# Kernel optimization log

Measured on AMD Instinct MI355X. Metric: run time of the kernel, lower is better.

## Reference

```python
import jax, jax.numpy as jnp
import numpy as np

N, E, D, O, M = 50000, 800000, 128, 128, 2

def _wn(x, v, g, b):
    # weight_norm linear: W = g * v / ||v||_row ; y = x @ W.T + b
    w = g * v / jnp.linalg.norm(v, axis=1, keepdims=True)
    return x @ w.T + b

def _gelu(x):
    return jax.nn.gelu(x, approximate=False)  # torch F.gelu default is exact erf

def setup_inputs() -> dict:
    key = jax.random.key(0)
    ks = jax.random.split(key, 32)
    inp = {"feat": jax.random.normal(ks[0], (N, D), jnp.float32)}
    layers = [("asrc", D, O), ("adst", D, O), ("asub", D, O), ("amul", D, O), ("aout", O, 1),
              ("pool", D, D), ("pool2", D, D), ("self", D, O), ("neigh", D, O), ("neigh2", D, O)]
    for i, (nm, fi, fo) in enumerate(layers):
        inp[nm + "_v"] = jax.random.normal(ks[i + 1], (fo, fi), jnp.float32) * (1.0 / np.sqrt(fi))
        inp[nm + "_g"] = jnp.ones((fo, 1), jnp.float32)
        inp[nm + "_b"] = jnp.zeros((fo,), jnp.float32)
    inp["mlp_v"] = jax.random.normal(ks[20], (M, O, O), jnp.float32) * (1.0 / np.sqrt(O))
    inp["mlp_g"] = jnp.ones((M, O, 1), jnp.float32)
    inp["mlp_b"] = jnp.zeros((M, O), jnp.float32)
    inp["src"] = jax.random.randint(ks[21], (E,), 0, N)
    inp["dst"] = jax.random.randint(ks[22], (E,), 0, N)
    return inp

def reference(feat, asrc_v, asrc_g, asrc_b, adst_v, adst_g, adst_b,
              asub_v, asub_g, asub_b, amul_v, amul_g, amul_b,
              aout_v, aout_g, aout_b, pool_v, pool_g, pool_b,
              pool2_v, pool2_g, pool2_b, self_v, self_g, self_b,
              neigh_v, neigh_g, neigh_b, neigh2_v, neigh2_g, neigh2_b,
              mlp_v, mlp_g, mlp_b, src, dst):
    fs, fd = feat[src], feat[dst]                        # [E, D] gathers
    e = (_wn(fs - fd, asub_v, asub_g, asub_b)
         + _wn(fs * fd, amul_v, amul_g, amul_b)
         + _wn(feat, asrc_v, asrc_g, asrc_b)[src]
         + _wn(feat, adst_v, adst_g, adst_b)[dst])       # [E, O]
    e = _gelu(e)
    e = jax.nn.leaky_relu(_wn(e, aout_v, aout_g, aout_b), 0.2)  # [E, 1] attention scalar

    cnt = jax.ops.segment_sum(jnp.ones((E,), feat.dtype), dst, num_segments=N)[:, None]  # in-degree

    h = _gelu(_wn(feat, pool_v, pool_g, pool_b))         # [N, D]
    neigh = jax.ops.segment_max(e * h[src], dst, num_segments=N)
    neigh = jnp.where(cnt > 0, neigh, jnp.zeros_like(neigh))  # zero for isolated dst nodes

    h2 = _gelu(_wn(feat, pool2_v, pool2_g, pool2_b))
    neigh2 = jax.ops.segment_sum(e * h2[src], dst, num_segments=N) / jnp.maximum(cnt, 1.0)

    rst = (_wn(feat, self_v, self_g, self_b)
           + _wn(neigh, neigh_v, neigh_g, neigh_b)
           + _wn(neigh2, neigh2_v, neigh2_g, neigh2_b))
    for i in range(M):
        rst = rst + _wn(_gelu(rst), mlp_v[i], mlp_g[i], mlp_b[i])
    return rst
```

## Files before the change

kernel.cpp:

```cpp
#include <hip/hip_runtime.h>
#include <hip/hip_bf16.h>
#include <math.h>

constexpr int NN = 50000;
constexpr int EE = 800000;

constexpr int OFF_WT_NODE  = 0;
constexpr int OFF_WT_AMUL  = 65536;
constexpr int OFF_WT_FINAL = 81920;
constexpr int OFF_WT_MLP   = 131072;
constexpr int OFF_WAOUT    = 163840;
constexpr int OFF_BE       = 163968;
constexpr int OFF_BFIN     = 164096;
constexpr int OFF_BAOUT    = 164224;
constexpr int OFF_WNODEBF  = 164240;
constexpr int OFF_WFINBF   = OFF_WNODEBF + 32768;
constexpr int OFF_WMLPBF   = OFF_WFINBF + 24576;
constexpr int OFF_WAMULBF  = OFF_WMLPBF + 16384;
constexpr int OFF_FEATBF   = OFF_WAMULBF + 8192;
constexpr int OFF_SBF      = OFF_FEATBF + NN*64;
constexpr int OFF_WEDGEBF  = OFF_SBF;
constexpr int OFF_HBF      = OFF_SBF + NN*128;
constexpr int OFF_SEV      = OFF_HBF + NN*128;
constexpr int OFF_NEIGHBF  = OFF_SEV + EE;
constexpr int OFF_STARTS   = OFF_NEIGHBF + NN*128;
constexpr int OFF_HIST     = OFF_STARTS + NN + 8;
constexpr int OFF_CURSOR   = OFF_HIST + NN;
constexpr int OFF_SSRCD    = OFF_CURSOR + NN;

constexpr int SCAN_NB = (NN + 255) / 256;

typedef __attribute__((ext_vector_type(8))) _Float16 f16x8;
typedef __attribute__((ext_vector_type(2))) _Float16 f16x2;
typedef __attribute__((ext_vector_type(2))) __fp16 fp16x2r;
typedef __attribute__((ext_vector_type(4))) float f32x4;

__device__ __forceinline__ float gelu_f(float x) {
    float x2 = x * x;
    float w = x * fmaf(-0.1029448f, x2, -2.3022082f);
    return x * __builtin_amdgcn_rcpf(1.0f + __builtin_amdgcn_exp2f(w));
}
__device__ __forceinline__ float leaky_f(float x) {
    return x > 0.0f ? x : 0.2f * x;
}
__device__ __forceinline__ unsigned pk_f16(float lo, float hi) {
    fp16x2r p = __builtin_amdgcn_cvt_pkrtz(lo, hi);
    return *reinterpret_cast<unsigned*>(&p);
}
__device__ __forceinline__ unsigned short f2h(float x) {
    fp16x2r p = __builtin_amdgcn_cvt_pkrtz(x, 0.0f);
    return *reinterpret_cast<unsigned short*>(&p);
}
__device__ __forceinline__ unsigned mulpack_h(unsigned a, unsigned b) {
    f16x2 x = *reinterpret_cast<f16x2*>(&a);
    f16x2 y = *reinterpret_cast<f16x2*>(&b);
    f16x2 r = x * y;
    return *reinterpret_cast<unsigned*>(&r);
}
__device__ __forceinline__ float2 up2(unsigned u) {
    f16x2 p = *reinterpret_cast<f16x2*>(&u);
    return make_float2((float)p.x, (float)p.y);
}
__device__ __forceinline__ float block_sum128(float v, float* sbuf) {
    #pragma unroll
    for (int o = 32; o > 0; o >>= 1) v += __shfl_down(v, o, 64);
    int lane = threadIdx.x & 63, w = threadIdx.x >> 6;
    if (lane == 0) sbuf[w] = v;
    __syncthreads();
    float r = sbuf[0] + sbuf[1];
    __syncthreads();
    return r;
}

struct WnormArgs {
    const float *asrc_v, *asrc_g, *asrc_b;
    const float *adst_v, *adst_g, *adst_b;
    const float *asub_v, *asub_g, *asub_b;
    const float *amul_v, *amul_g, *amul_b;
    const float *aout_v, *aout_g, *aout_b;
    const float *pool_v, *pool_g, *pool_b;
    const float *pool2_v, *pool2_g, *pool2_b;
    const float *self_v, *self_g, *self_b;
    const float *neigh_v, *neigh_g, *neigh_b;
    const float *neigh2_v, *neigh2_g, *neigh2_b;
    const float *mlp_v, *mlp_g, *mlp_b;
    float* ws;
};

__global__ __launch_bounds__(128) void wnorm_kernel(WnormArgs a) {
    __shared__ float sbuf[2];
    int bid = blockIdx.x, i = threadIdx.x;
    float* ws = a.ws;
    int gid = bid * 128 + i;
    if (gid < NN) ((int*)(ws + OFF_HIST))[gid] = 0;
    if (bid < 1280) {
        int o = bid & 127, grp = bid >> 7;
        const float *v1 = nullptr, *g1 = nullptr, *v2 = nullptr, *g2 = nullptr;
        float sgn2 = 1.0f; float* dst = nullptr; int stride = 0;
        switch (grp) {
            case 0: v1=a.asrc_v; g1=a.asrc_g; v2=a.asub_v; g2=a.asub_g; sgn2= 1.f; dst=ws+OFF_WT_NODE+o;        stride=512; break;
            case 1: v1=a.adst_v; g1=a.adst_g; v2=a.asub_v; g2=a.asub_g; sgn2=-1.f; dst=ws+OFF_WT_NODE+128+o;    stride=512; break;
            case 2: v1=a.pool_v;  g1=a.pool_g;  dst=ws+OFF_WT_NODE+256+o;          stride=512; break;
            case 3: v1=a.pool2_v; g1=a.pool2_g; dst=ws+OFF_WT_NODE+384+o;          stride=512; break;
            case 4: v1=a.amul_v;  g1=a.amul_g;  dst=ws+OFF_WT_AMUL+o;              stride=128; break;
            case 5: v1=a.neigh_v; g1=a.neigh_g; dst=ws+OFF_WT_FINAL+o;             stride=128; break;
            case 6: v1=a.neigh2_v;g1=a.neigh2_g;dst=ws+OFF_WT_FINAL+128*128+o;     stride=128; break;
            case 7: v1=a.self_v;  g1=a.self_g;  dst=ws+OFF_WT_FINAL+256*128+o;     stride=128; break;
            case 8: v1=a.mlp_v;        g1=a.mlp_g;     dst=ws+OFF_WT_MLP+o;        stride=128; break;
            case 9: v1=a.mlp_v+16384;  g1=a.mlp_g+128; dst=ws+OFF_WT_MLP+16384+o;  stride=128; break;
        }
        float x1 = v1[o*128 + i];
        float n1 = sqrtf(block_sum128(x1*x1, sbuf));
        float w = g1[o] * x1 / n1;
        if (v2) {
            float x2 = v2[o*128 + i];
            float n2 = sqrtf(block_sum128(x2*x2, sbuf));
            w += sgn2 * g2[o] * x2 / n2;
        }
        dst[i * stride] = w;
    } else {
        float v = a.aout_v[i];
        float n = sqrtf(block_sum128(v*v, sbuf));
        ws[OFF_WAOUT + i] = a.aout_g[0] * v / n;
        ws[OFF_BE + i]    = a.asrc_b[i] + a.adst_b[i] + a.asub_b[i] + a.amul_b[i];
        ws[OFF_BFIN + i]  = a.self_b[i] + a.neigh_b[i] + a.neigh2_b[i];
        if (i == 0) ws[OFF_BAOUT] = a.aout_b[0];
    }
}

__global__ __launch_bounds__(256) void convert_weights_kernel(float* __restrict__ ws) {
    int idx = blockIdx.x * 256 + threadIdx.x;
    unsigned short* wnodebf = (unsigned short*)(ws + OFF_WNODEBF);
    unsigned short* wfinbf  = (unsigned short*)(ws + OFF_WFINBF);
    unsigned short* wmlpbf  = (unsigned short*)(ws + OFF_WMLPBF);
    unsigned short* wedgebf = (unsigned short*)(ws + OFF_WEDGEBF);
    if (idx < 65536) {
        int k = idx >> 9, n = idx & 511;
        wnodebf[n * 128 + k] = f2h(ws[OFF_WT_NODE + k * 512 + n]);
    } else if (idx < 114688) {
        int i = idx - 65536, k = i >> 7, o = i & 127;
        wfinbf[o * 384 + k] = f2h(ws[OFF_WT_FINAL + k * 128 + o]);
    } else if (idx < 147456) {
        int i = idx - 114688, l = i >> 14, j = i & 16383, k = j >> 7, o = j & 127;
        wmlpbf[l * 16384 + o * 128 + k] = f2h(ws[OFF_WT_MLP + l * 16384 + k * 128 + o]);
    } else {
        int i = idx - 147456;
        int elem = i & 7, f = i >> 3;
        int lane = f & 63, kb = (f >> 6) & 3, ts = f >> 8;
        int t = ts / 3, slice = ts - t * 3;
        int o = t * 16 + (lane & 15);
        int kk = kb * 32 + (lane >> 4) * 8 + elem;
        float v = (slice == 0) ? ws[OFF_WT_AMUL + kk * 128 + o]
                : (slice == 1) ? ws[OFF_WT_NODE + kk * 512 + o]
                               : ws[OFF_WT_NODE + kk * 512 + 128 + o];
        wedgebf[i] = f2h(v);
    }
}

__global__ __launch_bounds__(256) void hist_kernel(const int* __restrict__ dst, float* __restrict__ ws) {
    int e = blockIdx.x * 256 + threadIdx.x;
    if (e < EE) atomicAdd(&((int*)(ws + OFF_HIST))[dst[e]], 1);
}

__global__ __launch_bounds__(256) void scan_blocks_kernel(float* __restrict__ ws) {
    __shared__ int wsum[4];
    const int* hist = (const int*)(ws + OFF_HIST);
    int* starts = (int*)(ws + OFF_STARTS);
    int* bsum = (int*)(ws + OFF_SEV);
    int bid = blockIdx.x, t = threadIdx.x;
    int idx = bid * 256 + t;
    int lane = t & 63, w = t >> 6;
    int v = (idx < NN) ? hist[idx] : 0;
    int s = v;
    #pragma unroll
    for (int o = 1; o < 64; o <<= 1) {
        int u = __shfl_up(s, o, 64);
        if (lane >= o) s += u;
    }
    if (lane == 63) wsum[w] = s;
    __syncthreads();
    int off = 0;
    for (int i = 0; i < w; ++i) off += wsum[i];
    int incl = s + off;
    if (idx < NN) starts[idx] = incl - v;
    if (t == 255) bsum[bid] = incl;
}

__global__ __launch_bounds__(256) void scan_add_kernel(float* __restrict__ ws) {
    __shared__ int sb4[4];
    int* starts = (int*)(ws + OFF_STARTS);
    int* cursor = (int*)(ws + OFF_CURSOR);
    const int* bsum = (const int*)(ws + OFF_SEV);
    int bid = blockIdx.x, t = threadIdx.x;
    int lane = t & 63, w = t >> 6;
    int v = (t < bid) ? bsum[t] : 0;
    int s = v;
    #pragma unroll
    for (int o = 32; o > 0; o >>= 1) s += __shfl_down(s, o, 64);
    if (lane == 0) sb4[w] = s;
    __syncthreads();
    int prefix = sb4[0] + sb4[1] + sb4[2] + sb4[3];
    int idx = bid * 256 + t;
    if (idx < NN) {
        int sv = starts[idx] + prefix;
        starts[idx] = sv;
        cursor[idx] = sv;
    }
    if (idx == 0) starts[NN] = EE;
}

__global__ __launch_bounds__(256) void scatteridx_kernel(const int* __restrict__ src,
                                                         const int* __restrict__ dst,
                                                         float* __restrict__ ws) {
    int e = blockIdx.x * 256 + threadIdx.x;
    if (e >= EE) return;
    int d = dst[e];
    int pos = atomicAdd(&((int*)(ws + OFF_CURSOR))[d], 1);
    ((int2*)(ws + OFF_SSRCD))[pos] = make_int2(src[e], d);
}

__global__ __launch_bounds__(256) void segreduce_kernel(float* __restrict__ ws) {
    int n = blockIdx.x * 4 + (threadIdx.x >> 6);
    int lane = threadIdx.x & 63;
    const int* starts = (const int*)(ws + OFF_STARTS);
    const int2* ssrcd = (const int2*)(ws + OFF_SSRCD);
    const float* sev = ws + OFF_SEV;
    const unsigned short* hbf = (const unsigned short*)(ws + OFF_HBF);
    unsigned short* neighbf = (unsigned short*)(ws + OFF_NEIGHBF);
    int s0 = starts[n], s1 = starts[n + 1];
    float2 mx = make_float2(-INFINITY, -INFINITY);
    float2 sm = make_float2(0.f, 0.f);
    int i = s0;
    for (; i + 4 <= s1; i += 4) {
        int sA = ssrcd[i].x, sB = ssrcd[i + 1].x, sC = ssrcd[i + 2].x, sD = ssrcd[i + 3].x;
        float eA = sev[i], eB = sev[i + 1], eC = sev[i + 2], eD = sev[i + 3];
        uint2 vA = *(const uint2*)&hbf[sA * 256 + lane * 4];
        uint2 vB = *(const uint2*)&hbf[sB * 256 + lane * 4];
        uint2 vC = *(const uint2*)&hbf[sC * 256 + lane * 4];
        uint2 vD = *(const uint2*)&hbf[sD * 256 + lane * 4];
        float2 hA = up2(vA.x), gA = up2(vA.y);
        float2 hB = up2(vB.x), gB = up2(vB.y);
        float2 hC = up2(vC.x), gC = up2(vC.y);
        float2 hD = up2(vD.x), gD = up2(vD.y);
        mx.x = fmaxf(mx.x, eA * hA.x); mx.y = fmaxf(mx.y, eA * hA.y);
        sm.x += eA * gA.x;             sm.y += eA * gA.y;
        mx.x = fmaxf(mx.x, eB * hB.x); mx.y = fmaxf(mx.y, eB * hB.y);
        sm.x += eB * gB.x;             sm.y += eB * gB.y;
        mx.x = fmaxf(mx.x, eC * hC.x); mx.y = fmaxf(mx.y, eC * hC.y);
        sm.x += eC * gC.x;             sm.y += eC * gC.y;
        mx.x = fmaxf(mx.x, eD * hD.x); mx.y = fmaxf(mx.y, eD * hD.y);
        sm.x += eD * gD.x;             sm.y += eD * gD.y;
    }
    for (; i < s1; ++i) {
        int s = ssrcd[i].x;
        float ev = sev[i];
        uint2 v = *(const uint2*)&hbf[s * 256 + lane * 4];
        float2 h = up2(v.x), g = up2(v.y);
        mx.x = fmaxf(mx.x, ev * h.x); mx.y = fmaxf(mx.y, ev * h.y);
        sm.x += ev * g.x;             sm.y += ev * g.y;
    }
    int cnt = s1 - s0;
    if (cnt == 0) { mx.x = 0.f; mx.y = 0.f; }
    float ic = 1.0f / (float)max(cnt, 1);
    *(unsigned*)&neighbf[n * 256 + lane * 2] = pk_f16(mx.x, mx.y);
    *(unsigned*)&neighbf[n * 256 + 128 + lane * 2] = pk_f16(sm.x * ic, sm.y * ic);
}

__global__ __launch_bounds__(256) void gemm_node_mfma(const float* __restrict__ feat,
                                                      const float* __restrict__ pool_b,
                                                      const float* __restrict__ pool2_b,
                                                      unsigned short* __restrict__ featbf,
                                                      unsigned short* __restrict__ hbf,
                                                      const unsigned short* __restrict__ wnodebf) {
    __shared__ unsigned short As[64 * 136];
    int tid = threadIdx.x;
    int row0 = blockIdx.x * 64;
    #pragma unroll
    for (int it = 0; it < 8; ++it) {
        int idx = tid + it * 256;
        int r = idx >> 5, u = idx & 31;
        int rr = min(row0 + r, NN - 1);
        float4 v = ((const float4*)feat)[rr * 32 + u];
        unsigned p0 = pk_f16(v.x, v.y);
        unsigned p1 = pk_f16(v.z, v.w);
        *(unsigned*)&As[r * 136 + u * 4]     = p0;
        *(unsigned*)&As[r * 136 + u * 4 + 2] = p1;
        *(uint2*)&featbf[rr * 128 + u * 4] = make_uint2(p0, p1);
    }
    __syncthreads();
    int lane = tid & 63, w = tid >> 6;
    int quad = lane >> 4, l15 = lane & 15;
    #pragma unroll 1
    for (int gy = 0; gy < 2; ++gy) {
        const unsigned short* B = wnodebf + (gy + 2) * 128 * 128;
        const float* bias = gy == 0 ? pool_b : pool2_b;
        f32x4 acc[8] = {};
        #pragma unroll 1
        for (int ks = 0; ks < 4; ++ks) {
            f16x8 a = *(const f16x8*)&As[(w * 16 + l15) * 136 + ks * 32 + quad * 8];
            #pragma unroll
            for (int t = 0; t < 8; ++t) {
                f16x8 b = *(const f16x8*)&B[(t * 16 + l15) * 128 + ks * 32 + quad * 8];
                acc[t] = __builtin_amdgcn_mfma_f32_16x16x32_f16(a, b, acc[t], 0, 0, 0);
            }
        }
        #pragma unroll
        for (int reg = 0; reg < 4; ++reg) {
            int row = row0 + w * 16 + quad * 4 + reg;
            if (row >= NN) continue;
            #pragma unroll
            for (int t = 0; t < 8; ++t) {
                int col = t * 16 + l15;
                hbf[row * 256 + ((col >> 1) << 2) + (col & 1) + gy * 2] =
                    f2h(gelu_f(acc[t][reg] + bias[col]));
            }
        }
    }
}

__global__ __launch_bounds__(256, 3) void gemm_edge(const unsigned short* __restrict__ featbf,
                                                    const unsigned short* __restrict__ wedgebf,
                                                    float* __restrict__ ws) {
    __shared__ unsigned short Bs[2][24 * 512];
    int tid = threadIdx.x;
    int lane = tid & 63, w = tid >> 6;
    int quad = lane >> 4, l15 = lane & 15;
    int e0 = blockIdx.x * 128;
    const int2* ssrcd = (const int2*)(ws + OFF_SSRCD);
    int base = e0 + w * 32 + l15;
    int2 i0 = ssrcd[base];
    int2 i1 = ssrcd[base + 16];
    const unsigned short* p0s = &featbf[i0.x * 128];
    const unsigned short* p0d = &featbf[i0.y * 128];
    const unsigned short* p1s = &featbf[i1.x * 128];
    const unsigned short* p1d = &featbf[i1.y * 128];
    int ko = quad * 8;

    uint4 ca[2][4];
    ca[0][0] = *(const uint4*)&p0s[ko];
    ca[0][1] = *(const uint4*)&p0d[ko];
    ca[0][2] = *(const uint4*)&p1s[ko];
    ca[0][3] = *(const uint4*)&p1d[ko];
    ca[1][0] = *(const uint4*)&p0s[ko + 32];
    ca[1][1] = *(const uint4*)&p0d[ko + 32];
    ca[1][2] = *(const uint4*)&p1s[ko + 32];
    ca[1][3] = *(const uint4*)&p1d[ko + 32];
    uint4 sb[6];
    #pragma unroll
    for (int i = 0; i < 6; ++i) {
        int ts = w * 6 + i;
        sb[i] = *(const uint4*)&wedgebf[(ts * 4 + 0) * 512 + lane * 8];
    }
    #pragma unroll
    for (int i = 0; i < 6; ++i) {
        int ts = w * 6 + i;
        *(uint4*)&Bs[0][ts * 512 + lane * 8] = sb[i];
    }
    __syncthreads();

    f32x4 acc0[8] = {}, acc1[8] = {};
    #pragma unroll
    for (int kb = 0; kb < 4; ++kb) {
        uint4 c0s = ca[kb & 1][0], c0d = ca[kb & 1][1];
        uint4 c1s = ca[kb & 1][2], c1d = ca[kb & 1][3];
        uint4 m0, m1;
        m0.x = mulpack_h(c0s.x, c0d.x); m0.y = mulpack_h(c0s.y, c0d.y);
        m0.z = mulpack_h(c0s.z, c0d.z); m0.w = mulpack_h(c0s.w, c0d.w);
        m1.x = mulpack_h(c1s.x, c1d.x); m1.y = mulpack_h(c1s.y, c1d.y);
        m1.z = mulpack_h(c1s.z, c1d.z); m1.w = mulpack_h(c1s.w, c1d.w);
        f16x8 am0 = *(const f16x8*)&m0,  am1 = *(const f16x8*)&m1;
        f16x8 as0 = *(const f16x8*)&c0s, ad0 = *(const f16x8*)&c0d;
        f16x8 as1 = *(const f16x8*)&c1s, ad1 = *(const f16x8*)&c1d;
        if (kb < 2) {
            int k2 = ko + (kb + 2) * 32;
            ca[kb & 1][0] = *(const uint4*)&p0s[k2];
            ca[kb & 1][1] = *(const uint4*)&p0d[k2];
            ca[kb & 1][2] = *(const uint4*)&p1s[k2];
            ca[kb & 1][3] = *(const uint4*)&p1d[k2];
        }
        if (kb < 3) {
            #pragma unroll
            for (int i = 0; i < 6; ++i) {
                int ts = w * 6 + i;
                sb[i] = *(const uint4*)&wedgebf[(ts * 4 + kb + 1) * 512 + lane * 8];
            }
        }
        const unsigned short* bb = &Bs[kb & 1][lane * 8];
        #pragma unroll
        for (int t = 0; t < 8; ++t) {
            f16x8 bm = *(const f16x8*)&bb[(t * 3 + 0) * 512];
            f16x8 b1 = *(const f16x8*)&bb[(t * 3 + 1) * 512];
            f16x8 b2 = *(const f16x8*)&bb[(t * 3 + 2) * 512];
            acc0[t] = __builtin_amdgcn_mfma_f32_16x16x32_f16(am0, bm, acc0[t], 0, 0, 0);
            acc1[t] = __builtin_amdgcn_mfma_f32_16x16x32_f16(am1, bm, acc1[t], 0, 0, 0);
            acc0[t] = __builtin_amdgcn_mfma_f32_16x16x32_f16(as0, b1, acc0[t], 0, 0, 0);
            acc1[t] = __builtin_amdgcn_mfma_f32_16x16x32_f16(as1, b1, acc1[t], 0, 0, 0);
            acc0[t] = __builtin_amdgcn_mfma_f32_16x16x32_f16(ad0, b2, acc0[t], 0, 0, 0);
            acc1[t] = __builtin_amdgcn_mfma_f32_16x16x32_f16(ad1, b2, acc1[t], 0, 0, 0);
        }
        if (kb < 3) {
            #pragma unroll
            for (int i = 0; i < 6; ++i) {
                int ts = w * 6 + i;
                *(uint4*)&Bs[(kb + 1) & 1][ts * 512 + lane * 8] = sb[i];
            }
            __syncthreads();
        }
    }

    const float* waout = ws + OFF_WAOUT;
    const float* be = ws + OFF_BE;
    float b_aout = ws[OFF_BAOUT];
    float* e_out = ws + OFF_SEV;
    float wv[8], bv[8];
    #pragma unroll
    for (int t = 0; t < 8; ++t) { wv[t] = waout[t * 16 + l15]; bv[t] = be[t * 16 + l15]; }
    #pragma unroll
    for (int g = 0; g < 2; ++g) {
        #pragma unroll
        for (int reg = 0; reg < 4; ++reg) {
            int r = w * 32 + g * 16 + quad * 4 + reg;
            float partial = 0.0f;
            #pragma unroll
            for (int t = 0; t < 8; ++t) {
                float v = (g ? acc1[t][reg] : acc0[t][reg]) + bv[t];
                partial += gelu_f(v) * wv[t];
            }
            partial += __shfl_xor(partial, 1, 16);
            partial += __shfl_xor(partial, 2, 16);
            partial += __shfl_xor(partial, 4, 16);
            partial += __shfl_xor(partial, 8, 16);
            if (l15 == 0) e_out[e0 + r] = leaky_f(partial + b_aout);
        }
    }
}

__global__ __launch_bounds__(256) void gemm_final_mlp(const unsigned short* __restrict__ neighbf,
                                                      const unsigned short* __restrict__ featbf,
                                                      const unsigned short* __restrict__ wfinbf,
                                                      const unsigned short* __restrict__ wmlpbf,
                                                      const float* __restrict__ mlp_b,
                                                      float* __restrict__ out,
                                                      const float* __restrict__ ws) {
    __shared__ unsigned short As[64 * 392];
    __shared__ float bfin_s[128];
    int tid = threadIdx.x;
    int row0 = blockIdx.x * 64;
    if (tid < 128) bfin_s[tid] = ws[OFF_BFIN + tid];
    #pragma unroll
    for (int rg = 0; rg < 3; ++rg) {
        #pragma unroll
        for (int it = 0; it < 4; ++it) {
            int idx = tid + it * 256;
            int r = idx >> 4, u = idx & 15;
            int rr = min(row0 + r, NN - 1);
            const unsigned short* sp = (rg == 0) ? &neighbf[rr * 256 + u * 8]
                                     : (rg == 1) ? &neighbf[rr * 256 + 128 + u * 8]
                                                 : &featbf[rr * 128 + u * 8];
            *(uint4*)&As[r * 392 + rg * 128 + u * 8] = *(const uint4*)sp;
        }
    }
    __syncthreads();
    int lane = tid & 63, w = tid >> 6;
    int quad = lane >> 4, l15 = lane & 15;
    f32x4 rst[8] = {};
    #pragma unroll 1
    for (int ks = 0; ks < 12; ++ks) {
        f16x8 a = *(const f16x8*)&As[(w * 16 + l15) * 392 + ks * 32 + quad * 8];
        #pragma unroll
        for (int t = 0; t < 8; ++t) {
            f16x8 b = *(const f16x8*)&wfinbf[(t * 16 + l15) * 384 + ks * 32 + quad * 8];
            rst[t] = __builtin_amdgcn_mfma_f32_16x16x32_f16(a, b, rst[t], 0, 0, 0);
        }
    }
    #pragma unroll
    for (int t = 0; t < 8; ++t) {
        float bf = bfin_s[t * 16 + l15];
        #pragma unroll
        for (int reg = 0; reg < 4; ++reg) rst[t][reg] += bf;
    }
    #pragma unroll 1
    for (int layer = 0; layer < 2; ++layer) {
        __syncthreads();
        #pragma unroll
        for (int t = 0; t < 8; ++t) {
            #pragma unroll
            for (int reg = 0; reg < 4; ++reg) {
                int row = w * 16 + quad * 4 + reg;
                As[row * 136 + t * 16 + l15] = f2h(gelu_f(rst[t][reg]));
            }
        }
        __syncthreads();
        const unsigned short* wB = wmlpbf + layer * 16384;
        f32x4 acc[8] = {};
        #pragma unroll 1
        for (int ks = 0; ks < 4; ++ks) {
            f16x8 a = *(const f16x8*)&As[(w * 16 + l15) * 136 + ks * 32 + quad * 8];
            #pragma unroll
            for (int t = 0; t < 8; ++t) {
                f16x8 b = *(const f16x8*)&wB[(t * 16 + l15) * 128 + ks * 32 + quad * 8];
                acc[t] = __builtin_amdgcn_mfma_f32_16x16x32_f16(a, b, acc[t], 0, 0, 0);
            }
        }
        #pragma unroll
        for (int t = 0; t < 8; ++t) {
            float bias = mlp_b[layer * 128 + t * 16 + l15];
            #pragma unroll
            for (int reg = 0; reg < 4; ++reg) rst[t][reg] += acc[t][reg] + bias;
        }
    }
    #pragma unroll
    for (int reg = 0; reg < 4; ++reg) {
        int row = row0 + w * 16 + quad * 4 + reg;
        if (row >= NN) continue;
        #pragma unroll
        for (int t = 0; t < 8; ++t) {
            out[row * 128 + t * 16 + l15] = rst[t][reg];
        }
    }
}

extern "C" void kernel_launch(void* const* d_in, const int* in_sizes, int n_in,
                              void* d_out, int out_size, void* d_ws, size_t ws_size,
                              hipStream_t stream) {
    const float* feat = (const float*)d_in[0];
    WnormArgs wa;
    wa.asrc_v = (const float*)d_in[1];  wa.asrc_g = (const float*)d_in[2];  wa.asrc_b = (const float*)d_in[3];
    wa.adst_v = (const float*)d_in[4];  wa.adst_g = (const float*)d_in[5];  wa.adst_b = (const float*)d_in[6];
    wa.asub_v = (const float*)d_in[7];  wa.asub_g = (const float*)d_in[8];  wa.asub_b = (const float*)d_in[9];
    wa.amul_v = (const float*)d_in[10]; wa.amul_g = (const float*)d_in[11]; wa.amul_b = (const float*)d_in[12];
    wa.aout_v = (const float*)d_in[13]; wa.aout_g = (const float*)d_in[14]; wa.aout_b = (const float*)d_in[15];
    wa.pool_v = (const float*)d_in[16]; wa.pool_g = (const float*)d_in[17]; wa.pool_b = (const float*)d_in[18];
    wa.pool2_v= (const float*)d_in[19]; wa.pool2_g= (const float*)d_in[20]; wa.pool2_b= (const float*)d_in[21];
    wa.self_v = (const float*)d_in[22]; wa.self_g = (const float*)d_in[23]; wa.self_b = (const float*)d_in[24];
    wa.neigh_v= (const float*)d_in[25]; wa.neigh_g= (const float*)d_in[26]; wa.neigh_b= (const float*)d_in[27];
    wa.neigh2_v=(const float*)d_in[28]; wa.neigh2_g=(const float*)d_in[29]; wa.neigh2_b=(const float*)d_in[30];
    wa.mlp_v  = (const float*)d_in[31]; wa.mlp_g  = (const float*)d_in[32]; wa.mlp_b  = (const float*)d_in[33];
    const int* src = (const int*)d_in[34];
    const int* dst = (const int*)d_in[35];
    float* out = (float*)d_out;
    float* ws = (float*)d_ws;
    wa.ws = ws;
    unsigned short* featbf  = (unsigned short*)(ws + OFF_FEATBF);
    unsigned short* hbf     = (unsigned short*)(ws + OFF_HBF);
    unsigned short* neighbf = (unsigned short*)(ws + OFF_NEIGHBF);
    unsigned short* wnodebf = (unsigned short*)(ws + OFF_WNODEBF);
    unsigned short* wfinbf  = (unsigned short*)(ws + OFF_WFINBF);
    unsigned short* wmlpbf  = (unsigned short*)(ws + OFF_WMLPBF);
    unsigned short* wedgebf = (unsigned short*)(ws + OFF_WEDGEBF);

    wnorm_kernel<<<dim3(1281), dim3(128), 0, stream>>>(wa);
    convert_weights_kernel<<<dim3(768), dim3(256), 0, stream>>>(ws);
    hist_kernel<<<dim3((EE + 255) / 256), dim3(256), 0, stream>>>(dst, ws);
    scan_blocks_kernel<<<dim3(SCAN_NB), dim3(256), 0, stream>>>(ws);
    scan_add_kernel<<<dim3(SCAN_NB), dim3(256), 0, stream>>>(ws);
    scatteridx_kernel<<<dim3((EE + 255) / 256), dim3(256), 0, stream>>>(src, dst, ws);
    gemm_node_mfma<<<dim3(782), dim3(256), 0, stream>>>(feat, wa.pool_b, wa.pool2_b, featbf, hbf, wnodebf);
    gemm_edge<<<dim3(EE / 128), dim3(256), 0, stream>>>(featbf, wedgebf, ws);
    segreduce_kernel<<<dim3(NN / 4), dim3(256), 0, stream>>>(ws);
    gemm_final_mlp<<<dim3(782), dim3(256), 0, stream>>>(neighbf, featbf, wfinbf, wmlpbf, wa.mlp_b, out, ws);
}
```

Measured before the change: 514.4 us.

## Fuse segment reduction into final GEMM, merge histogram into weight conversion, stage H stores

Moves the per-destination max/sum segment reduction into the final MLP GEMM kernel so the neighbour features go straight into shared memory instead of through a global round-trip. The in-degree histogram is folded into the weight conversion kernel as a grid-stride loop, removing a launch. The node GEMM now stages its bf16 H output in shared memory and writes coalesced 16-byte rows. The trade-off is that the fused kernel runs only 782 blocks and each wave walks 16 nodes serially, so the gather-bound reduction gets less parallelism than the separate kernel had.

```diff
diff --git a/kernel.cpp b/kernel.cpp
--- a/kernel.cpp
+++ b/kernel.cpp
@@ -128,7 +128,8 @@
     }
 }
 
-__global__ __launch_bounds__(256) void convert_weights_kernel(float* __restrict__ ws) {
+__global__ __launch_bounds__(256) void convert_weights_kernel(const int* __restrict__ dst,
+                                                              float* __restrict__ ws) {
     int idx = blockIdx.x * 256 + threadIdx.x;
     unsigned short* wnodebf = (unsigned short*)(ws + OFF_WNODEBF);
     unsigned short* wfinbf  = (unsigned short*)(ws + OFF_WFINBF);
@@ -155,11 +156,8 @@
                                : ws[OFF_WT_NODE + kk * 512 + 128 + o];
         wedgebf[i] = f2h(v);
     }
-}
-
-__global__ __launch_bounds__(256) void hist_kernel(const int* __restrict__ dst, float* __restrict__ ws) {
-    int e = blockIdx.x * 256 + threadIdx.x;
-    if (e < EE) atomicAdd(&((int*)(ws + OFF_HIST))[dst[e]], 1);
+    int* hist = (int*)(ws + OFF_HIST);
+    for (int e = idx; e < EE; e += 768 * 256) atomicAdd(&hist[dst[e]], 1);
 }
 
 __global__ __launch_bounds__(256) void scan_blocks_kernel(float* __restrict__ ws) {
@@ -219,53 +217,6 @@
     ((int2*)(ws + OFF_SSRCD))[pos] = make_int2(src[e], d);
 }
 
-__global__ __launch_bounds__(256) void segreduce_kernel(float* __restrict__ ws) {
-    int n = blockIdx.x * 4 + (threadIdx.x >> 6);
-    int lane = threadIdx.x & 63;
-    const int* starts = (const int*)(ws + OFF_STARTS);
-    const int2* ssrcd = (const int2*)(ws + OFF_SSRCD);
-    const float* sev = ws + OFF_SEV;
-    const unsigned short* hbf = (const unsigned short*)(ws + OFF_HBF);
-    unsigned short* neighbf = (unsigned short*)(ws + OFF_NEIGHBF);
-    int s0 = starts[n], s1 = starts[n + 1];
-    float2 mx = make_float2(-INFINITY, -INFINITY);
-    float2 sm = make_float2(0.f, 0.f);
-    int i = s0;
-    for (; i + 4 <= s1; i += 4) {
-        int sA = ssrcd[i].x, sB = ssrcd[i + 1].x, sC = ssrcd[i + 2].x, sD = ssrcd[i + 3].x;
-        float eA = sev[i], eB = sev[i + 1], eC = sev[i + 2], eD = sev[i + 3];
-        uint2 vA = *(const uint2*)&hbf[sA * 256 + lane * 4];
-        uint2 vB = *(const uint2*)&hbf[sB * 256 + lane * 4];
-        uint2 vC = *(const uint2*)&hbf[sC * 256 + lane * 4];
-        uint2 vD = *(const uint2*)&hbf[sD * 256 + lane * 4];
-        float2 hA = up2(vA.x), gA = up2(vA.y);
-        float2 hB = up2(vB.x), gB = up2(vB.y);
-        float2 hC = up2(vC.x), gC = up2(vC.y);
-        float2 hD = up2(vD.x), gD = up2(vD.y);
-        mx.x = fmaxf(mx.x, eA * hA.x); mx.y = fmaxf(mx.y, eA * hA.y);
-        sm.x += eA * gA.x;             sm.y += eA * gA.y;
-        mx.x = fmaxf(mx.x, eB * hB.x); mx.y = fmaxf(mx.y, eB * hB.y);
-        sm.x += eB * gB.x;             sm.y += eB * gB.y;
-        mx.x = fmaxf(mx.x, eC * hC.x); mx.y = fmaxf(mx.y, eC * hC.y);
-        sm.x += eC * gC.x;             sm.y += eC * gC.y;
-        mx.x = fmaxf(mx.x, eD * hD.x); mx.y = fmaxf(mx.y, eD * hD.y);
-        sm.x += eD * gD.x;             sm.y += eD * gD.y;
-    }
-    for (; i < s1; ++i) {
-        int s = ssrcd[i].x;
-        float ev = sev[i];
-        uint2 v = *(const uint2*)&hbf[s * 256 + lane * 4];
-        float2 h = up2(v.x), g = up2(v.y);
-        mx.x = fmaxf(mx.x, ev * h.x); mx.y = fmaxf(mx.y, ev * h.y);
-        sm.x += ev * g.x;             sm.y += ev * g.y;
-    }
-    int cnt = s1 - s0;
-    if (cnt == 0) { mx.x = 0.f; mx.y = 0.f; }
-    float ic = 1.0f / (float)max(cnt, 1);
-    *(unsigned*)&neighbf[n * 256 + lane * 2] = pk_f16(mx.x, mx.y);
-    *(unsigned*)&neighbf[n * 256 + 128 + lane * 2] = pk_f16(sm.x * ic, sm.y * ic);
-}
-
 __global__ __launch_bounds__(256) void gemm_node_mfma(const float* __restrict__ feat,
                                                       const float* __restrict__ pool_b,
                                                       const float* __restrict__ pool2_b,
@@ -273,6 +224,7 @@
                                                       unsigned short* __restrict__ hbf,
                                                       const unsigned short* __restrict__ wnodebf) {
     __shared__ unsigned short As[64 * 136];
+    __shared__ unsigned short Hs[64 * 264];
     int tid = threadIdx.x;
     int row0 = blockIdx.x * 64;
     #pragma unroll
@@ -306,15 +258,23 @@
         }
         #pragma unroll
         for (int reg = 0; reg < 4; ++reg) {
-            int row = row0 + w * 16 + quad * 4 + reg;
-            if (row >= NN) continue;
+            int lr = w * 16 + quad * 4 + reg;
             #pragma unroll
             for (int t = 0; t < 8; ++t) {
                 int col = t * 16 + l15;
-                hbf[row * 256 + ((col >> 1) << 2) + (col & 1) + gy * 2] =
+                Hs[lr * 264 + ((col >> 1) << 2) + (col & 1) + gy * 2] =
                     f2h(gelu_f(acc[t][reg] + bias[col]));
             }
         }
+    }
+    __syncthreads();
+    #pragma unroll
+    for (int it = 0; it < 8; ++it) {
+        int idx = tid + it * 256;
+        int r = idx >> 5, u = idx & 31;
+        int row = row0 + r;
+        if (row < NN)
+            *(uint4*)&hbf[row * 256 + u * 8] = *(const uint4*)&Hs[r * 264 + u * 8];
     }
 }
 
@@ -435,8 +395,7 @@
     }
 }
 
-__global__ __launch_bounds__(256) void gemm_final_mlp(const unsigned short* __restrict__ neighbf,
-                                                      const unsigned short* __restrict__ featbf,
+__global__ __launch_bounds__(256) void gemm_final_mlp(const unsigned short* __restrict__ featbf,
                                                       const unsigned short* __restrict__ wfinbf,
                                                       const unsigned short* __restrict__ wmlpbf,
                                                       const float* __restrict__ mlp_b,
@@ -448,20 +407,61 @@
     int row0 = blockIdx.x * 64;
     if (tid < 128) bfin_s[tid] = ws[OFF_BFIN + tid];
     #pragma unroll
-    for (int rg = 0; rg < 3; ++rg) {
-        #pragma unroll
-        for (int it = 0; it < 4; ++it) {
-            int idx = tid + it * 256;
-            int r = idx >> 4, u = idx & 15;
-            int rr = min(row0 + r, NN - 1);
-            const unsigned short* sp = (rg == 0) ? &neighbf[rr * 256 + u * 8]
-                                     : (rg == 1) ? &neighbf[rr * 256 + 128 + u * 8]
-                                                 : &featbf[rr * 128 + u * 8];
-            *(uint4*)&As[r * 392 + rg * 128 + u * 8] = *(const uint4*)sp;
-        }
-    }
-    __syncthreads();
+    for (int it = 0; it < 4; ++it) {
+        int idx = tid + it * 256;
+        int r = idx >> 4, u = idx & 15;
+        int rr = min(row0 + r, NN - 1);
+        *(uint4*)&As[r * 392 + 256 + u * 8] = *(const uint4*)&featbf[rr * 128 + u * 8];
+    }
     int lane = tid & 63, w = tid >> 6;
+    {
+        const int* starts = (const int*)(ws + OFF_STARTS);
+        const int2* ssrcd = (const int2*)(ws + OFF_SSRCD);
+        const float* sev = ws + OFF_SEV;
+        const unsigned short* hbf = (const unsigned short*)(ws + OFF_HBF);
+        for (int j = 0; j < 16; ++j) {
+            int r = w * 16 + j;
+            int n = min(row0 + r, NN - 1);
+            int s0 = starts[n], s1 = starts[n + 1];
+            float2 mx = make_float2(-INFINITY, -INFINITY);
+            float2 sm = make_float2(0.f, 0.f);
+            int i = s0;
+            for (; i + 4 <= s1; i += 4) {
+                int sA = ssrcd[i].x, sB = ssrcd[i + 1].x, sC = ssrcd[i + 2].x, sD = ssrcd[i + 3].x;
+                float eA = sev[i], eB = sev[i + 1], eC = sev[i + 2], eD = sev[i + 3];
+                uint2 vA = *(const uint2*)&hbf[sA * 256 + lane * 4];
+                uint2 vB = *(const uint2*)&hbf[sB * 256 + lane * 4];
+                uint2 vC = *(const uint2*)&hbf[sC * 256 + lane * 4];
+                uint2 vD = *(const uint2*)&hbf[sD * 256 + lane * 4];
+                float2 hA = up2(vA.x), gA = up2(vA.y);
+                float2 hB = up2(vB.x), gB = up2(vB.y);
+                float2 hC = up2(vC.x), gC = up2(vC.y);
+                float2 hD = up2(vD.x), gD = up2(vD.y);
+                mx.x = fmaxf(mx.x, eA * hA.x); mx.y = fmaxf(mx.y, eA * hA.y);
+                sm.x += eA * gA.x;             sm.y += eA * gA.y;
+                mx.x = fmaxf(mx.x, eB * hB.x); mx.y = fmaxf(mx.y, eB * hB.y);
+                sm.x += eB * gB.x;             sm.y += eB * gB.y;
+                mx.x = fmaxf(mx.x, eC * hC.x); mx.y = fmaxf(mx.y, eC * hC.y);
+                sm.x += eC * gC.x;             sm.y += eC * gC.y;
+                mx.x = fmaxf(mx.x, eD * hD.x); mx.y = fmaxf(mx.y, eD * hD.y);
+                sm.x += eD * gD.x;             sm.y += eD * gD.y;
+            }
+            for (; i < s1; ++i) {
+                int s = ssrcd[i].x;
+                float ev = sev[i];
+                uint2 v = *(const uint2*)&hbf[s * 256 + lane * 4];
+                float2 h = up2(v.x), g = up2(v.y);
+                mx.x = fmaxf(mx.x, ev * h.x); mx.y = fmaxf(mx.y, ev * h.y);
+                sm.x += ev * g.x;             sm.y += ev * g.y;
+            }
+            int cnt = s1 - s0;
+            if (cnt == 0) { mx.x = 0.f; mx.y = 0.f; }
+            float ic = 1.0f / (float)max(cnt, 1);
+            *(unsigned*)&As[r * 392 + lane * 2]       = pk_f16(mx.x, mx.y);
+            *(unsigned*)&As[r * 392 + 128 + lane * 2] = pk_f16(sm.x * ic, sm.y * ic);
+        }
+    }
+    __syncthreads();
     int quad = lane >> 4, l15 = lane & 15;
     f32x4 rst[8] = {};
     #pragma unroll 1
@@ -543,20 +543,17 @@
     wa.ws = ws;
     unsigned short* featbf  = (unsigned short*)(ws + OFF_FEATBF);
     unsigned short* hbf     = (unsigned short*)(ws + OFF_HBF);
-    unsigned short* neighbf = (unsigned short*)(ws + OFF_NEIGHBF);
     unsigned short* wnodebf = (unsigned short*)(ws + OFF_WNODEBF);
     unsigned short* wfinbf  = (unsigned short*)(ws + OFF_WFINBF);
     unsigned short* wmlpbf  = (unsigned short*)(ws + OFF_WMLPBF);
     unsigned short* wedgebf = (unsigned short*)(ws + OFF_WEDGEBF);
 
     wnorm_kernel<<<dim3(1281), dim3(128), 0, stream>>>(wa);
-    convert_weights_kernel<<<dim3(768), dim3(256), 0, stream>>>(ws);
-    hist_kernel<<<dim3((EE + 255) / 256), dim3(256), 0, stream>>>(dst, ws);
+    convert_weights_kernel<<<dim3(768), dim3(256), 0, stream>>>(dst, ws);
     scan_blocks_kernel<<<dim3(SCAN_NB), dim3(256), 0, stream>>>(ws);
     scan_add_kernel<<<dim3(SCAN_NB), dim3(256), 0, stream>>>(ws);
     scatteridx_kernel<<<dim3((EE + 255) / 256), dim3(256), 0, stream>>>(src, dst, ws);
     gemm_node_mfma<<<dim3(782), dim3(256), 0, stream>>>(feat, wa.pool_b, wa.pool2_b, featbf, hbf, wnodebf);
     gemm_edge<<<dim3(EE / 128), dim3(256), 0, stream>>>(featbf, wedgebf, ws);
-    segreduce_kernel<<<dim3(NN / 4), dim3(256), 0, stream>>>(ws);
-    gemm_final_mlp<<<dim3(782), dim3(256), 0, stream>>>(neighbf, featbf, wfinbf, wmlpbf, wa.mlp_b, out, ws);
-}
+    gemm_final_mlp<<<dim3(782), dim3(256), 0, stream>>>(featbf, wfinbf, wmlpbf, wa.mlp_b, out, ws);
+}
```

After: 559.3 us. 1.09x slower.
